# Kernel tuning notes

Measured on AMD Instinct MI355X. Metric: run time of the kernel, lower is better.

## Reference

```python
import jax, jax.numpy as jnp
import numpy as np


def setup_inputs() -> dict:
    key = jax.random.key(0)
    k_w, k_e = jax.random.split(key)
    NUM_EDGE_TYPES = 8
    NUM_CHANNELS = 4
    NUM_NODES = 4096
    NUM_EDGES = 262144  # per edge type, avg degree 64
    weights = jax.random.normal(k_w, (NUM_CHANNELS, NUM_EDGE_TYPES), dtype=jnp.float32)
    edge_index = jax.random.randint(k_e, (NUM_EDGE_TYPES, 2, NUM_EDGES), 0, NUM_NODES, dtype=jnp.int64)
    return {"weights": weights, "edge_index": edge_index, "num_nodes": NUM_NODES}


def reference(weights, edge_index, num_nodes):
    # to_dense_adj: scatter-add ones into an [N, N] dense adjacency per edge type
    def dense_adj(ei):  # ei: [2, num_edges]
        A = jnp.zeros((num_nodes, num_nodes), dtype=jnp.float32)
        return A.at[ei[0], ei[1]].add(1.0)

    A_stack = jax.vmap(dense_adj)(edge_index)          # [E, N, N]
    soft_weights = jax.nn.softmax(weights, axis=-1)    # [C, E]
    A_meta = jnp.einsum('ce,enm->cnm', soft_weights, A_stack)  # [C, N, N]
    return A_meta, soft_weights
```

## Files before the change

kernel.cpp:

```cpp
#include <hip/hip_runtime.h>

#define N_NODES   4096
#define NUM_ET    8
#define NUM_CH    4
#define NUM_EDGES 262144
#define NN        ((size_t)N_NODES * N_NODES)
#define A_SIZE    (NUM_CH * NN)

#define NGROUPS     2048
#define P1_BLOCKS   256
#define P1_THREADS  1024
#define EDGES_PER_BLOCK (NUM_ET * NUM_EDGES / P1_BLOCKS)
#define CHUNKS_PER_TYPE (NUM_EDGES / EDGES_PER_BLOCK)
#define SLOT_CAP    15
#define REG_U16     16
#define OVF_CAP     16384

typedef float vfloat4 __attribute__((ext_vector_type(4)));

__global__ __launch_bounds__(P1_THREADS) void bin_edges(
        const int* __restrict__ ei,
        unsigned short* __restrict__ slots,
        unsigned int* __restrict__ ovf_cnt,
        unsigned int* __restrict__ ovf) {
    __shared__ unsigned short sslot[NGROUPS * REG_U16];
    __shared__ unsigned int   lcnt[NGROUPS];
    const int t   = threadIdx.x;
    const int blk = blockIdx.x;

    for (int g = t; g < NGROUPS; g += P1_THREADS) lcnt[g] = 0;
    __syncthreads();

    const int e     = blk / CHUNKS_PER_TYPE;
    const int chunk = blk % CHUNKS_PER_TYPE;
    const int* srcb = ei + (size_t)(2 * e) * NUM_EDGES + chunk * EDGES_PER_BLOCK;
    const int* dstb = srcb + NUM_EDGES;
    const unsigned tag = (unsigned)e << 12;

    #pragma unroll
    for (int j = 0; j < EDGES_PER_BLOCK / (4 * P1_THREADS); ++j) {
        int off = j * (4 * P1_THREADS) + t * 4;
        int4 s4 = *(const int4*)(srcb + off);
        int4 d4 = *(const int4*)(dstb + off);
        int ss[4] = {s4.x, s4.y, s4.z, s4.w};
        int dd[4] = {d4.x, d4.y, d4.z, d4.w};
        #pragma unroll
        for (int k = 0; k < 4; ++k) {
            int g = ss[k] >> 1;
            unsigned rec = ((unsigned)(ss[k] & 1) << 15) | tag | (unsigned)dd[k];
            unsigned pos = atomicAdd(&lcnt[g], 1u);
            if (pos < SLOT_CAP) {
                sslot[g * REG_U16 + pos] = (unsigned short)rec;
            } else {
                unsigned ix = atomicAdd(ovf_cnt, 1u);
                if (ix < OVF_CAP) ovf[ix] = ((unsigned)g << 16) | rec;
            }
        }
    }
    __syncthreads();

    for (int g = t; g < NGROUPS; g += P1_THREADS) {
        uint4 a = *(const uint4*)&sslot[g * REG_U16];
        uint4 b = *(const uint4*)&sslot[g * REG_U16 + 8];
        unsigned c = min(lcnt[g], (unsigned)SLOT_CAP);
        b.w = (b.w & 0xFFFFu) | (c << 16);
        uint4* dp = (uint4*)(slots + ((size_t)blk * NGROUPS + g) * REG_U16);
        dp[0] = a;
        dp[1] = b;
    }
}

__global__ __launch_bounds__(256) void expand_quads(
        const float* __restrict__ w,
        const unsigned short* __restrict__ slots,
        const unsigned int* __restrict__ ovf_cnt,
        const unsigned int* __restrict__ ovf,
        float* __restrict__ out) {
    __shared__ unsigned int cnt[4 * N_NODES];
    __shared__ float swl_s[NUM_CH * NUM_ET];
    const int t = threadIdx.x;
    const int G = blockIdx.x;

    const uint4* rp = (const uint4*)(slots + ((size_t)t * NGROUPS + 2 * G) * REG_U16);
    uint4 q0 = rp[0];
    uint4 q1 = rp[1];
    uint4 q2 = rp[2];
    uint4 q3 = rp[3];

    for (int i = t; i < 4 * N_NODES; i += 256) cnt[i] = 0;
    if (t < NUM_CH) {
        float v[NUM_ET];
        float m = -1e30f;
        #pragma unroll
        for (int e = 0; e < NUM_ET; ++e) {
            v[e] = w[t * NUM_ET + e];
            m = fmaxf(m, v[e]);
        }
        float s = 0.0f;
        #pragma unroll
        for (int e = 0; e < NUM_ET; ++e) { v[e] = expf(v[e] - m); s += v[e]; }
        float inv = 1.0f / s;
        #pragma unroll
        for (int e = 0; e < NUM_ET; ++e) swl_s[t * NUM_ET + e] = v[e] * inv;
    }
    __syncthreads();

    #pragma unroll
    for (int h = 0; h < 2; ++h) {
        uint4 qa = h ? q2 : q0;
        uint4 qb = h ? q3 : q1;
        int n = (int)(qb.w >> 16);
        unsigned su[8] = {qa.x, qa.y, qa.z, qa.w, qb.x, qb.y, qb.z, qb.w};
        #pragma unroll
        for (int wd = 0; wd < 8; ++wd) {
            int b2 = 2 * wd;
            if (b2 < n) {
                unsigned v = su[wd] & 0xFFFFu;
                atomicAdd(&cnt[((2 * h + (int)(v >> 15)) << 12) + (v & 4095u)],
                          1u << (4 * ((v >> 12) & 7u)));
                if (b2 + 1 < n) {
                    v = su[wd] >> 16;
                    atomicAdd(&cnt[((2 * h + (int)(v >> 15)) << 12) + (v & 4095u)],
                              1u << (4 * ((v >> 12) & 7u)));
                }
            }
        }
    }
    unsigned novf = min(*ovf_cnt, (unsigned)OVF_CAP);
    for (unsigned i = t; i < novf; i += 256) {
        unsigned r32 = ovf[i];
        unsigned g = r32 >> 16;
        if ((int)(g >> 1) == G) {
            unsigned v = r32 & 0xFFFFu;
            int row_local = (int)((g & 1u) << 1) + (int)(v >> 15);
            atomicAdd(&cnt[(row_local << 12) + (v & 4095u)],
                      1u << (4 * ((v >> 12) & 7u)));
        }
    }
    __syncthreads();

    float swl[NUM_CH][NUM_ET];
    #pragma unroll
    for (int c = 0; c < NUM_CH; ++c)
        #pragma unroll
        for (int e = 0; e < NUM_ET; ++e)
            swl[c][e] = swl_s[c * NUM_ET + e];

    #pragma unroll
    for (int r1 = 0; r1 < 4; ++r1) {
        const size_t rowbase = (size_t)(4 * G + r1) * N_NODES;
        #pragma unroll
        for (int j = 0; j < 4; ++j) {
            int cell = j * 1024 + t * 4;
            uint4 wq = *(const uint4*)&cnt[(r1 << 12) + cell];
            unsigned wk[4] = {wq.x, wq.y, wq.z, wq.w};
            float o[NUM_CH][4];
            #pragma unroll
            for (int k = 0; k < 4; ++k) {
                float a0 = 0.f, a1 = 0.f, a2 = 0.f, a3 = 0.f;
                #pragma unroll
                for (int e = 0; e < NUM_ET; ++e) {
                    float f = (float)((wk[k] >> (4 * e)) & 0xFu);
                    a0 += swl[0][e] * f;
                    a1 += swl[1][e] * f;
                    a2 += swl[2][e] * f;
                    a3 += swl[3][e] * f;
                }
                o[0][k] = a0; o[1][k] = a1; o[2][k] = a2; o[3][k] = a3;
            }
            #pragma unroll
            for (int c = 0; c < NUM_CH; ++c) {
                vfloat4 v4 = {o[c][0], o[c][1], o[c][2], o[c][3]};
                __builtin_nontemporal_store(
                    v4, (vfloat4*)(out + (size_t)c * NN + rowbase + cell));
            }
        }
    }

    if (G == 0 && t < NUM_CH * NUM_ET) out[A_SIZE + t] = swl_s[t];
}

extern "C" void kernel_launch(void* const* d_in, const int* in_sizes, int n_in,
                              void* d_out, int out_size, void* d_ws, size_t ws_size,
                              hipStream_t stream) {
    const float* weights = (const float*)d_in[0];
    const int*   ei      = (const int*)d_in[1];
    float* out = (float*)d_out;

    char* ws = (char*)d_ws;
    unsigned short* slots   = (unsigned short*)ws;
    size_t slots_bytes      = (size_t)P1_BLOCKS * NGROUPS * REG_U16 * sizeof(unsigned short);
    unsigned int*   ovf_cnt = (unsigned int*)(ws + slots_bytes);
    unsigned int*   ovf     = ovf_cnt + 64;

    hipMemsetAsync(ovf_cnt, 0, sizeof(unsigned int), stream);
    bin_edges<<<P1_BLOCKS, P1_THREADS, 0, stream>>>(ei, slots, ovf_cnt, ovf);
    expand_quads<<<N_NODES / 4, 256, 0, stream>>>(weights, slots, ovf_cnt, ovf, out);
}
```

Measured before the change: 298.1 us.

## Use per-block overflow lists and 512-thread expand blocks, drop memset

```diff
diff --git a/kernel.cpp b/kernel.cpp
--- a/kernel.cpp
+++ b/kernel.cpp
@@ -14,21 +14,22 @@
 #define CHUNKS_PER_TYPE (NUM_EDGES / EDGES_PER_BLOCK)
 #define SLOT_CAP    15
 #define REG_U16     16
-#define OVF_CAP     16384
+#define OVF_PER_BLK 64
 
 typedef float vfloat4 __attribute__((ext_vector_type(4)));
 
 __global__ __launch_bounds__(P1_THREADS) void bin_edges(
         const int* __restrict__ ei,
         unsigned short* __restrict__ slots,
-        unsigned int* __restrict__ ovf_cnt,
         unsigned int* __restrict__ ovf) {
     __shared__ unsigned short sslot[NGROUPS * REG_U16];
     __shared__ unsigned int   lcnt[NGROUPS];
+    __shared__ unsigned int   lovf;
     const int t   = threadIdx.x;
     const int blk = blockIdx.x;
 
     for (int g = t; g < NGROUPS; g += P1_THREADS) lcnt[g] = 0;
+    if (t == 0) lovf = 0;
     __syncthreads();
 
     const int e     = blk / CHUNKS_PER_TYPE;
@@ -36,6 +37,7 @@
     const int* srcb = ei + (size_t)(2 * e) * NUM_EDGES + chunk * EDGES_PER_BLOCK;
     const int* dstb = srcb + NUM_EDGES;
     const unsigned tag = (unsigned)e << 12;
+    unsigned int* myovf = ovf + blk * OVF_PER_BLK;
 
     #pragma unroll
     for (int j = 0; j < EDGES_PER_BLOCK / (4 * P1_THREADS); ++j) {
@@ -52,12 +54,14 @@
             if (pos < SLOT_CAP) {
                 sslot[g * REG_U16 + pos] = (unsigned short)rec;
             } else {
-                unsigned ix = atomicAdd(ovf_cnt, 1u);
-                if (ix < OVF_CAP) ovf[ix] = ((unsigned)g << 16) | rec;
-            }
-        }
-    }
-    __syncthreads();
+                unsigned ix = atomicAdd(&lovf, 1u);
+                if (ix < OVF_PER_BLK - 1)
+                    myovf[1 + ix] = ((unsigned)g << 16) | rec;
+            }
+        }
+    }
+    __syncthreads();
+    if (t == 0) myovf[0] = min(lovf, (unsigned)(OVF_PER_BLK - 1));
 
     for (int g = t; g < NGROUPS; g += P1_THREADS) {
         uint4 a = *(const uint4*)&sslot[g * REG_U16];
@@ -70,24 +74,29 @@
     }
 }
 
-__global__ __launch_bounds__(256) void expand_quads(
+__global__ __launch_bounds__(512) void expand_quads(
         const float* __restrict__ w,
         const unsigned short* __restrict__ slots,
-        const unsigned int* __restrict__ ovf_cnt,
         const unsigned int* __restrict__ ovf,
         float* __restrict__ out) {
     __shared__ unsigned int cnt[4 * N_NODES];
     __shared__ float swl_s[NUM_CH * NUM_ET];
     const int t = threadIdx.x;
     const int G = blockIdx.x;
-
-    const uint4* rp = (const uint4*)(slots + ((size_t)t * NGROUPS + 2 * G) * REG_U16);
-    uint4 q0 = rp[0];
-    uint4 q1 = rp[1];
-    uint4 q2 = rp[2];
-    uint4 q3 = rp[3];
-
-    for (int i = t; i < 4 * N_NODES; i += 256) cnt[i] = 0;
+    const int bb = t >> 1;
+    const int gh = t & 1;
+
+    const uint4* rp = (const uint4*)(slots +
+        ((size_t)bb * NGROUPS + 2 * G + gh) * REG_U16);
+    uint4 qa = rp[0];
+    uint4 qb = rp[1];
+
+    {
+        uint4 z = {0u, 0u, 0u, 0u};
+        uint4* cz = (uint4*)cnt;
+        #pragma unroll
+        for (int i = 0; i < 8; ++i) cz[i * 512 + t] = z;
+    }
     if (t < NUM_CH) {
         float v[NUM_ET];
         float m = -1e30f;
@@ -105,36 +114,37 @@
     }
     __syncthreads();
 
-    #pragma unroll
-    for (int h = 0; h < 2; ++h) {
-        uint4 qa = h ? q2 : q0;
-        uint4 qb = h ? q3 : q1;
+    {
         int n = (int)(qb.w >> 16);
+        int base = gh << 1;
         unsigned su[8] = {qa.x, qa.y, qa.z, qa.w, qb.x, qb.y, qb.z, qb.w};
         #pragma unroll
         for (int wd = 0; wd < 8; ++wd) {
             int b2 = 2 * wd;
             if (b2 < n) {
                 unsigned v = su[wd] & 0xFFFFu;
-                atomicAdd(&cnt[((2 * h + (int)(v >> 15)) << 12) + (v & 4095u)],
+                atomicAdd(&cnt[((base + (int)(v >> 15)) << 12) + (v & 4095u)],
                           1u << (4 * ((v >> 12) & 7u)));
                 if (b2 + 1 < n) {
                     v = su[wd] >> 16;
-                    atomicAdd(&cnt[((2 * h + (int)(v >> 15)) << 12) + (v & 4095u)],
+                    atomicAdd(&cnt[((base + (int)(v >> 15)) << 12) + (v & 4095u)],
                               1u << (4 * ((v >> 12) & 7u)));
                 }
             }
         }
     }
-    unsigned novf = min(*ovf_cnt, (unsigned)OVF_CAP);
-    for (unsigned i = t; i < novf; i += 256) {
-        unsigned r32 = ovf[i];
-        unsigned g = r32 >> 16;
-        if ((int)(g >> 1) == G) {
-            unsigned v = r32 & 0xFFFFu;
-            int row_local = (int)((g & 1u) << 1) + (int)(v >> 15);
-            atomicAdd(&cnt[(row_local << 12) + (v & 4095u)],
-                      1u << (4 * ((v >> 12) & 7u)));
+    if (t < P1_BLOCKS) {
+        const unsigned int* mo = ovf + t * OVF_PER_BLK;
+        unsigned n = mo[0];
+        for (unsigned j = 0; j < n; ++j) {
+            unsigned r32 = mo[1 + j];
+            unsigned g = r32 >> 16;
+            if ((int)(g >> 1) == G) {
+                unsigned v = r32 & 0xFFFFu;
+                int row_local = (int)((g & 1u) << 1) + (int)(v >> 15);
+                atomicAdd(&cnt[(row_local << 12) + (v & 4095u)],
+                          1u << (4 * ((v >> 12) & 7u)));
+            }
         }
     }
     __syncthreads();
@@ -150,8 +160,8 @@
     for (int r1 = 0; r1 < 4; ++r1) {
         const size_t rowbase = (size_t)(4 * G + r1) * N_NODES;
         #pragma unroll
-        for (int j = 0; j < 4; ++j) {
-            int cell = j * 1024 + t * 4;
+        for (int j = 0; j < 2; ++j) {
+            int cell = j * 2048 + t * 4;
             uint4 wq = *(const uint4*)&cnt[(r1 << 12) + cell];
             unsigned wk[4] = {wq.x, wq.y, wq.z, wq.w};
             float o[NUM_CH][4];
@@ -188,12 +198,10 @@
     float* out = (float*)d_out;
 
     char* ws = (char*)d_ws;
-    unsigned short* slots   = (unsigned short*)ws;
-    size_t slots_bytes      = (size_t)P1_BLOCKS * NGROUPS * REG_U16 * sizeof(unsigned short);
-    unsigned int*   ovf_cnt = (unsigned int*)(ws + slots_bytes);
-    unsigned int*   ovf     = ovf_cnt + 64;
-
-    hipMemsetAsync(ovf_cnt, 0, sizeof(unsigned int), stream);
-    bin_edges<<<P1_BLOCKS, P1_THREADS, 0, stream>>>(ei, slots, ovf_cnt, ovf);
-    expand_quads<<<N_NODES / 4, 256, 0, stream>>>(weights, slots, ovf_cnt, ovf, out);
+    unsigned short* slots = (unsigned short*)ws;
+    size_t slots_bytes    = (size_t)P1_BLOCKS * NGROUPS * REG_U16 * sizeof(unsigned short);
+    unsigned int*   ovf   = (unsigned int*)(ws + slots_bytes);
+
+    bin_edges<<<P1_BLOCKS, P1_THREADS, 0, stream>>>(ei, slots, ovf);
+    expand_quads<<<N_NODES / 4, 512, 0, stream>>>(weights, slots, ovf, out);
 }
```

After: 293.6 us. About the same (-1.5%).
